# Optimization experiments

Measured on AMD Instinct MI355X. Metric: run time of the kernel, lower is better.

Reference implementation:

```python
import jax, jax.numpy as jnp
import numpy as np

B, S, D = 4, 8192, 512
WS = 512        # window_size
LB = 1          # look_backward (look_forward = 0, causal)


def setup_inputs() -> dict:
    key = jax.random.key(0)
    k1, k2, k3 = jax.random.split(key, 3)
    text = jax.random.normal(k1, (B, S, D), dtype=jnp.float32)
    audio = jax.random.normal(k2, (B, S, D), dtype=jnp.float32)
    video = jax.random.normal(k3, (B, S, D), dtype=jnp.float32)
    return {"text": text, "audio": audio, "video": video}


def _local_attention(q, k, v, ws=WS, lb=LB):
    # q, k, v: [b, n, d]; sliding-window causal attention, each query window
    # attends to its own window plus `lb` previous windows.
    b, n, d = q.shape
    w = n // ws
    scale = d ** -0.5
    qw = q.reshape(b, w, ws, d) * scale
    kw = k.reshape(b, w, ws, d)
    vw = v.reshape(b, w, ws, d)

    def look_around(x):
        # pad lb windows of zeros at the front, gather lb+1 shifted views
        padded = jnp.pad(x, ((0, 0), (lb, 0), (0, 0), (0, 0)))
        return jnp.concatenate([padded[:, i:i + w] for i in range(lb + 1)], axis=2)

    kk = look_around(kw)  # [b, w, (lb+1)*ws, d]
    vv = look_around(vw)

    # absolute positions for causal + padding mask
    t = jnp.arange(n).reshape(w, ws)                        # query positions [w, ws]
    tk = jnp.pad(t, ((lb, 0), (0, 0)), constant_values=-1)  # pad windows get -1
    bq_k = jnp.concatenate([tk[i:i + w] for i in range(lb + 1)], axis=1)  # [w, (lb+1)*ws]
    mask = (t[:, :, None] >= bq_k[:, None, :]) & (bq_k[:, None, :] >= 0)  # [w, ws, (lb+1)*ws]

    sim = jnp.einsum('bwid,bwjd->bwij', qw, kk)             # [b, w, ws, (lb+1)*ws]
    sim = jnp.where(mask[None], sim, jnp.finfo(sim.dtype).min)
    attn = jax.nn.softmax(sim, axis=-1)
    out = jnp.einsum('bwij,bwjd->bwid', attn, vv)
    return out.reshape(b, n, d)


def reference(text, audio, video):
    # GATSBlock.forward: x = self.local_attn(text, audio, video)
    # i.e. q = text, k = audio, v = video (modalities pre-projected to [b, n, d])
    return _local_attention(text, audio, video)
```

## Files before the change

kernel.cpp:

```cpp
#include <hip/hip_runtime.h>
#include <hip/hip_bf16.h>

#define S_ 8192
#define D_ 512
#define WSZ 512
#define QBLK 128
#define KBLK 32
#define ATT_THREADS 512
#define PREG 131072
#define PSTRIDE 2560
#define ATT_LDS (PREG + 4 * PSTRIDE)

using bf16x8 = __attribute__((ext_vector_type(8))) __bf16;
using f32x4  = __attribute__((ext_vector_type(4))) float;
using f32x16 = __attribute__((ext_vector_type(16))) float;

#define GLDS(gp, lp) __builtin_amdgcn_global_load_lds( \
    (const __attribute__((address_space(1))) void*)(gp), \
    (__attribute__((address_space(3))) void*)(lp), 16, 0, 0)

__global__ __launch_bounds__(256) void cvt_k(const float* __restrict__ in,
                                             ushort* __restrict__ out) {
    const int bid = blockIdx.x;
    const int j = bid & 7, t = (bid >> 3) & 255, b = bid >> 11;
    const int u = j * 256 + threadIdx.x;
    const int c = u >> 7, row = (u >> 2) & 31, h = u & 3;
    const float* src = in + ((size_t)(b * S_ + t * 32 + row)) * D_ + c * 32 + h * 8;
    float4 a0 = *(const float4*)(src);
    float4 a1 = *(const float4*)(src + 4);
    bf16x8 o;
    o[0] = (__bf16)a0.x; o[1] = (__bf16)a0.y; o[2] = (__bf16)a0.z; o[3] = (__bf16)a0.w;
    o[4] = (__bf16)a1.x; o[5] = (__bf16)a1.y; o[6] = (__bf16)a1.z; o[7] = (__bf16)a1.w;
    *(bf16x8*)(out + (size_t)(b * 256 + t) * 16384 + u * 8) = o;
}

__global__ __launch_bounds__(256) void tr_v(const float* __restrict__ V,
                                            char* __restrict__ Vt) {
    __shared__ float tile[64][68];
    const int bid = blockIdx.x;
    const int d0 = (bid & 7) * 64;
    const int s0 = ((bid >> 3) & 127) * 64;
    const int b  = bid >> 10;
    const int t  = threadIdx.x;
    {
        const int sl = t >> 2, cg = (t & 3) * 16;
        const float* src = V + ((size_t)b * S_ + s0 + sl) * D_ + d0 + cg;
        #pragma unroll
        for (int j = 0; j < 4; ++j)
            *(float4*)&tile[sl][cg + j * 4] = *(const float4*)(src + j * 4);
    }
    __syncthreads();
    {
        const int dl = t >> 2, sg = (t & 3) * 16;
        const int d  = d0 + dl;
        const int tt = (s0 + sg) >> 5;
        const int kk = (s0 + sg) & 31;
        bf16x8 o0, o1;
        #pragma unroll
        for (int j = 0; j < 8; ++j) {
            o0[j] = (__bf16)tile[sg + j][dl];
            o1[j] = (__bf16)tile[sg + 8 + j][dl];
        }
        char* base = Vt + (size_t)(b * 256 + tt) * 32768 +
                     (d >> 5) * 2048 + (d & 31) * 16;
        *(bf16x8*)(base + (kk >> 4) * 1024)       = o0;
        *(bf16x8*)(base + (kk >> 4) * 1024 + 512) = o1;
    }
}

__global__ __launch_bounds__(ATT_THREADS, 2) void gats_attn(
    const float* __restrict__ Qg, const char* __restrict__ Kbg,
    const char* __restrict__ Vtg, float* __restrict__ Og)
{
    extern __shared__ char smem[];
    const int tid  = threadIdx.x;
    const int lane = tid & 63;
    const int wv   = tid >> 6;
    const int h    = lane >> 4;
    const int lq   = lane & 15;
    const int hh   = lane >> 5;
    const int l31  = lane & 31;
    const int u    = wv & 1;
    const int pr   = wv >> 1;
    char* Pp = smem + PREG + pr * PSTRIDE;
    char* Pf = Pp + 2048;
    const int laneK = lq * 64 + h * 16;

    const int bid = blockIdx.x;
    const int r2  = bid >> 3;
    const int w   = (bid & 7) * 2 + (r2 & 1);
    const int b   = (r2 >> 1) & 3;
    const int y   = r2 >> 3;
    const int qbase    = w * WSZ + y * QBLK;
    const int pairbase = qbase + pr * 32;
    const int wqbase   = qbase + wv * 16;

    const float* Qp  = Qg  + (size_t)b * S_ * D_;
    const char*  Kbp = Kbg + (size_t)b * 256 * 32768;
    const char*  Vtp = Vtg + (size_t)b * 256 * 32768;
    float*       Op  = Og  + (size_t)b * S_ * D_;

    const float scale = 0.044194173824159216f;
    const float L2E   = 1.44269504088896f;

    bf16x8 qf[16];
    {
        const int qrow = wqbase + lq;
        const float* qsrc = Qp + (size_t)qrow * D_ + h * 8;
        #pragma unroll
        for (int c = 0; c < 16; ++c) {
            float4 a0 = *(const float4*)(qsrc + c * 32);
            float4 a1 = *(const float4*)(qsrc + c * 32 + 4);
            bf16x8 q;
            q[0] = (__bf16)(a0.x * scale); q[1] = (__bf16)(a0.y * scale);
            q[2] = (__bf16)(a0.z * scale); q[3] = (__bf16)(a0.w * scale);
            q[4] = (__bf16)(a1.x * scale); q[5] = (__bf16)(a1.y * scale);
            q[6] = (__bf16)(a1.z * scale); q[7] = (__bf16)(a1.w * scale);
            qf[c] = q;
        }
    }

    f32x16 acc[8];
    #pragma unroll
    for (int dt = 0; dt < 8; ++dt)
        #pragma unroll
        for (int rg = 0; rg < 16; ++rg) acc[dt][rg] = 0.f;
    float m_run = -1e30f, l_run = 0.f;

    const int kstart = (w == 0) ? 0 : (w - 1) * WSZ;
    const int ktend  = qbase + QBLK;

    auto STAGE = [&](int bufi, int kt) {
        char* kb = smem + bufi * 65536;
        char* vb = kb + 32768;
        const size_t tb = ((size_t)(kt >> 5)) << 15;
        const char* ksrc = Kbp + tb;
        const char* vsrc = Vtp + tb;
        #pragma unroll
        for (int s2 = 0; s2 < 4; ++s2) {
            const int off = wv * 4096 + s2 * 1024;
            GLDS(ksrc + off + lane * 16, kb + off);
            GLDS(vsrc + off + lane * 16, vb + off);
        }
    };

    STAGE(0, kstart);
    int cur = 0;
    for (int kt = kstart; kt < ktend; kt += KBLK) {
        const bool hasnext = (kt + KBLK) < ktend;
        if (hasnext) {
            STAGE(cur ^ 1, kt + KBLK);
            asm volatile("s_waitcnt vmcnt(8)" ::: "memory");
        } else {
            asm volatile("s_waitcnt vmcnt(0)" ::: "memory");
        }
        __builtin_amdgcn_s_barrier();

        const bool active = (kt <= pairbase + 31);
        char* Ksh = smem + cur * 65536;
        char* Vsh = Ksh + 32768;

        if (active) {
            f32x4 st[2];
            __builtin_amdgcn_s_setprio(1);
            #pragma unroll
            for (int g = 0; g < 2; ++g) {
                f32x4 sa = (f32x4){0.f, 0.f, 0.f, 0.f};
                f32x4 sb = (f32x4){0.f, 0.f, 0.f, 0.f};
                #pragma unroll
                for (int c = 0; c < 16; ++c) {
                    const int byte = c * 2048 + g * 1024 + laneK;
                    bf16x8 kf = *(const bf16x8*)(Ksh + byte);
                    if (c & 1) sb = __builtin_amdgcn_mfma_f32_16x16x32_bf16(kf, qf[c], sb, 0, 0, 0);
                    else       sa = __builtin_amdgcn_mfma_f32_16x16x32_bf16(kf, qf[c], sa, 0, 0, 0);
                }
                st[g] = sa + sb;
            }
            __builtin_amdgcn_s_setprio(0);

            const int qg = wqbase + lq;
            if (kt + 31 > wqbase) {
                #pragma unroll
                for (int g = 0; g < 2; ++g)
                    #pragma unroll
                    for (int r = 0; r < 4; ++r) {
                        const int key = kt + g * 16 + h * 4 + r;
                        if (key > qg) st[g][r] = -1e30f;
                    }
            }

            float own = fmaxf(fmaxf(fmaxf(st[0][0], st[0][1]), fmaxf(st[0][2], st[0][3])),
                              fmaxf(fmaxf(st[1][0], st[1][1]), fmaxf(st[1][2], st[1][3])));
            float tmax = fmaxf(own, __shfl_xor(own, 16));
            tmax = fmaxf(tmax, __shfl_xor(tmax, 32));

            const bool anyneed = __any(tmax > m_run + 8.f);
            float f_val = 1.0f;
            if (anyneed) {
                const float mnew = fmaxf(m_run, tmax);
                f_val = exp2f((m_run - mnew) * L2E);
                m_run = mnew;
                l_run *= f_val;
            }

            const float p00 = exp2f((st[0][0] - m_run) * L2E);
            const float p01 = exp2f((st[0][1] - m_run) * L2E);
            const float p02 = exp2f((st[0][2] - m_run) * L2E);
            const float p03 = exp2f((st[0][3] - m_run) * L2E);
            const float p10 = exp2f((st[1][0] - m_run) * L2E);
            const float p11 = exp2f((st[1][1] - m_run) * L2E);
            const float p12 = exp2f((st[1][2] - m_run) * L2E);
            const float p13 = exp2f((st[1][3] - m_run) * L2E);
            float rs = p00 + p01 + p02 + p03 + p10 + p11 + p12 + p13;
            rs += __shfl_xor(rs, 16);
            rs += __shfl_xor(rs, 32);
            l_run += rs;

            uint c0, c1, c2, c3;
            asm("v_cvt_pk_bf16_f32 %0, %1, %2" : "=v"(c0) : "v"(p00), "v"(p01));
            asm("v_cvt_pk_bf16_f32 %0, %1, %2" : "=v"(c1) : "v"(p02), "v"(p03));
            asm("v_cvt_pk_bf16_f32 %0, %1, %2" : "=v"(c2) : "v"(p10), "v"(p11));
            asm("v_cvt_pk_bf16_f32 %0, %1, %2" : "=v"(c3) : "v"(p12), "v"(p13));
            const int wbase = (h >> 1) * 512 + (h & 1) * 8 + (u * 16 + lq) * 16;
            *(uint*)(Pp + wbase)            = c0;
            *(uint*)(Pp + wbase + 4)        = c1;
            *(uint*)(Pp + 1024 + wbase)     = c2;
            *(uint*)(Pp + 1024 + wbase + 4) = c3;
            if (h == 0)    *(float*)(Pf + (u * 16 + lq) * 4) = f_val;
            if (lane == 0) *(uint*)(Pf + 128 + u * 4) = anyneed ? 1u : 0u;
        }

        asm volatile("s_waitcnt lgkmcnt(0)" ::: "memory");
        __builtin_amdgcn_sched_barrier(0);
        __builtin_amdgcn_s_barrier();

        if (active) {
            const uint2 fl = *(const uint2*)(Pf + 128);
            if (fl.x | fl.y) {
                f32x4 fr[4];
                #pragma unroll
                for (int i = 0; i < 4; ++i)
                    fr[i] = *(const f32x4*)(Pf + i * 32 + hh * 16);
                #pragma unroll
                for (int dt = 0; dt < 8; ++dt)
                    #pragma unroll
                    for (int rg = 0; rg < 16; ++rg)
                        acc[dt][rg] *= fr[rg >> 2][rg & 3];
            }

            bf16x8 pa0 = *(const bf16x8*)(Pp + hh * 512 + l31 * 16);
            bf16x8 pa1 = *(const bf16x8*)(Pp + 1024 + hh * 512 + l31 * 16);
            __builtin_amdgcn_s_setprio(1);
            #pragma unroll
            for (int dt = 0; dt < 8; ++dt) {
                const int vb = (u * 8 + dt) * 2048 + hh * 512 + l31 * 16;
                bf16x8 v0 = *(const bf16x8*)(Vsh + vb);
                bf16x8 v1 = *(const bf16x8*)(Vsh + vb + 1024);
                acc[dt] = __builtin_amdgcn_mfma_f32_32x32x16_bf16(pa0, v0, acc[dt], 0, 0, 0);
                acc[dt] = __builtin_amdgcn_mfma_f32_32x32x16_bf16(pa1, v1, acc[dt], 0, 0, 0);
            }
            __builtin_amdgcn_s_setprio(0);
        }
        __builtin_amdgcn_s_barrier();
        cur ^= 1;
    }

    if (h == 0) *(float*)(Pf + (u * 16 + lq) * 4) = l_run;
    asm volatile("s_waitcnt lgkmcnt(0)" ::: "memory");
    __builtin_amdgcn_s_barrier();
    f32x4 iv[4];
    #pragma unroll
    for (int i = 0; i < 4; ++i) {
        f32x4 lv = *(const f32x4*)(Pf + i * 32 + hh * 16);
        iv[i][0] = 1.0f / lv[0]; iv[i][1] = 1.0f / lv[1];
        iv[i][2] = 1.0f / lv[2]; iv[i][3] = 1.0f / lv[3];
    }
    #pragma unroll
    for (int dt = 0; dt < 8; ++dt) {
        const int colb = u * 256 + dt * 32 + l31;
        #pragma unroll
        for (int rg = 0; rg < 16; ++rg) {
            const int row = pairbase + (rg & 3) + 8 * (rg >> 2) + 4 * hh;
            Op[(size_t)row * D_ + colb] = acc[dt][rg] * iv[rg >> 2][rg & 3];
        }
    }
}

#define FB_LDS (32768 + 32768 + 4 * 1024)
__global__ __launch_bounds__(256, 2) void gats_attn_fb(
    const float* __restrict__ Qg, const float* __restrict__ Kg,
    const float* __restrict__ Vg, float* __restrict__ Og)
{
    extern __shared__ char smem[];
    char* Ksh = smem;
    char* Vsh = smem + 32768;
    const int tid  = threadIdx.x;
    const int lane = tid & 63;
    const int wv   = tid >> 6;
    char* Psh = smem + 65536 + wv * 1024;
    const int bid = blockIdx.x;
    const int wh  = bid & 7;
    const int r2  = bid >> 3;
    const int w   = wh * 2 + (r2 & 1);
    const int b   = (r2 >> 1) & 3;
    const int y   = r2 >> 3;
    const int qbase  = w * WSZ + y * 64;
    const int wqbase = qbase + wv * 16;
    const size_t boff = (size_t)b * S_ * D_;
    const float* Qp = Qg + boff; const float* Kp = Kg + boff;
    const float* Vp = Vg + boff; float* Op = Og + boff;
    const float scale = 0.044194173824159216f;
    const float L2E   = 1.44269504088896f;
    bf16x8 qf[16];
    {
        const int qrow = wqbase + (lane & 15);
        const float* qsrc = Qp + (size_t)qrow * D_ + ((lane >> 4) * 8);
        #pragma unroll
        for (int c = 0; c < 16; ++c) {
            float4 a0 = *(const float4*)(qsrc + c * 32);
            float4 a1 = *(const float4*)(qsrc + c * 32 + 4);
            bf16x8 q;
            q[0] = (__bf16)(a0.x * scale); q[1] = (__bf16)(a0.y * scale);
            q[2] = (__bf16)(a0.z * scale); q[3] = (__bf16)(a0.w * scale);
            q[4] = (__bf16)(a1.x * scale); q[5] = (__bf16)(a1.y * scale);
            q[6] = (__bf16)(a1.z * scale); q[7] = (__bf16)(a1.w * scale);
            qf[c] = q;
        }
    }
    f32x4 acc[32];
    #pragma unroll
    for (int i = 0; i < 32; ++i) acc[i] = (f32x4){0.f, 0.f, 0.f, 0.f};
    float m_r[4], l_r[4];
    #pragma unroll
    for (int r = 0; r < 4; ++r) { m_r[r] = -1e30f; l_r[r] = 0.f; }
    const int kstart = (w == 0) ? 0 : (w - 1) * WSZ;
    const int ktend  = qbase + 64;
    for (int kt = kstart; kt < ktend; kt += 32) {
        __syncthreads();
        #pragma unroll
        for (int s = 0; s < 8; ++s) {
            const int row = s * 4 + wv;
            const int dof = lane * 8;
            const float4* src = (const float4*)(Kp + (size_t)(kt + row) * D_ + dof);
            float4 a0 = src[0], a1 = src[1];
            bf16x8 kv;
            kv[0] = (__bf16)a0.x; kv[1] = (__bf16)a0.y; kv[2] = (__bf16)a0.z; kv[3] = (__bf16)a0.w;
            kv[4] = (__bf16)a1.x; kv[5] = (__bf16)a1.y; kv[6] = (__bf16)a1.z; kv[7] = (__bf16)a1.w;
            const int byte = row * 1024 + ((dof * 2) ^ ((row & 7) << 4));
            *(bf16x8*)(Ksh + byte) = kv;
        }
        #pragma unroll
        for (int hh2 = 0; hh2 < 2; ++hh2) {
            const int d = tid + hh2 * 256;
            #pragma unroll
            for (int it = 0; it < 4; ++it) {
                float vvv[8];
                #pragma unroll
                for (int j = 0; j < 8; ++j)
                    vvv[j] = Vp[(size_t)(kt + it * 8 + j) * D_ + d];
                bf16x8 vb;
                #pragma unroll
                for (int j = 0; j < 8; ++j) vb[j] = (__bf16)vvv[j];
                const int byte = d * 64 + ((it * 16) ^ (((d >> 1) & 3) << 4));
                *(bf16x8*)(Vsh + byte) = vb;
            }
        }
        __syncthreads();
        if (kt > wqbase + 15) continue;
        f32x4 sacc[2];
        #pragma unroll
        for (int g = 0; g < 2; ++g) {
            f32x4 s = (f32x4){0.f, 0.f, 0.f, 0.f};
            const int keyrow = g * 16 + (lane & 15);
            #pragma unroll
            for (int c = 0; c < 16; ++c) {
                const int byte = keyrow * 1024 +
                                 ((c * 64 + (lane >> 4) * 16) ^ ((keyrow & 7) << 4));
                bf16x8 kf = *(const bf16x8*)(Ksh + byte);
                s = __builtin_amdgcn_mfma_f32_16x16x32_bf16(qf[c], kf, s, 0, 0, 0);
            }
            sacc[g] = s;
        }
        #pragma unroll
        for (int g = 0; g < 2; ++g) {
            if (kt + g * 16 + 15 > wqbase) {
                const int kg = kt + g * 16 + (lane & 15);
                #pragma unroll
                for (int r = 0; r < 4; ++r) {
                    const int qrow = wqbase + (lane >> 4) * 4 + r;
                    if (kg > qrow) sacc[g][r] = -1e30f;
                }
            }
        }
        float tmax[4];
        #pragma unroll
        for (int r = 0; r < 4; ++r) {
            float v = fmaxf(sacc[0][r], sacc[1][r]);
            #pragma unroll
            for (int off = 8; off >= 1; off >>= 1)
                v = fmaxf(v, __shfl_xor(v, off));
            tmax[r] = v;
        }
        bool need = false;
        #pragma unroll
        for (int r = 0; r < 4; ++r) need |= (tmax[r] > m_r[r] + 8.f);
        if (__any(need)) {
            #pragma unroll
            for (int r = 0; r < 4; ++r) {
                const float mnew = fmaxf(m_r[r], tmax[r]);
                const float f = exp2f((m_r[r] - mnew) * L2E);
                m_r[r] = mnew; l_r[r] *= f;
                #pragma unroll
                for (int dc = 0; dc < 32; ++dc) acc[dc][r] *= f;
            }
        }
        float rsum[4] = {0.f, 0.f, 0.f, 0.f};
        #pragma unroll
        for (int g = 0; g < 2; ++g) {
            #pragma unroll
            for (int r = 0; r < 4; ++r) {
                const float p = exp2f((sacc[g][r] - m_r[r]) * L2E);
                rsum[r] += p;
                const int prow = (lane >> 4) * 4 + r;
                const int byte = prow * 64 +
                                 ((g * 32 + (lane & 15) * 2) ^ (((prow >> 1) & 3) << 4));
                *(__bf16*)(Psh + byte) = (__bf16)p;
            }
        }
        #pragma unroll
        for (int r = 0; r < 4; ++r) {
            float v = rsum[r];
            #pragma unroll
            for (int off = 8; off >= 1; off >>= 1)
                v += __shfl_xor(v, off);
            l_r[r] += v;
        }
        {
            const int prow  = lane & 15;
            const int pbyte = prow * 64 +
                              (((lane >> 4) * 16) ^ (((prow >> 1) & 3) << 4));
            bf16x8 pa = *(const bf16x8*)(Psh + pbyte);
            #pragma unroll
            for (int dc = 0; dc < 32; ++dc) {
                const int d = dc * 16 + (lane & 15);
                const int vbyte = d * 64 +
                                  (((lane >> 4) * 16) ^ (((d >> 1) & 3) << 4));
                bf16x8 vf = *(const bf16x8*)(Vsh + vbyte);
                acc[dc] = __builtin_amdgcn_mfma_f32_16x16x32_bf16(pa, vf, acc[dc], 0, 0, 0);
            }
        }
    }
    float inv[4];
    #pragma unroll
    for (int r = 0; r < 4; ++r) inv[r] = 1.0f / l_r[r];
    #pragma unroll
    for (int dc = 0; dc < 32; ++dc) {
        #pragma unroll
        for (int r = 0; r < 4; ++r) {
            const int row = wqbase + (lane >> 4) * 4 + r;
            const int col = dc * 16 + (lane & 15);
            Op[(size_t)row * D_ + col] = acc[dc][r] * inv[r];
        }
    }
}

extern "C" void kernel_launch(void* const* d_in, const int* in_sizes, int n_in,
                              void* d_out, int out_size, void* d_ws, size_t ws_size,
                              hipStream_t stream) {
    const float* q = (const float*)d_in[0];
    const float* k = (const float*)d_in[1];
    const float* v = (const float*)d_in[2];
    float* o = (float*)d_out;

    const size_t elems = (size_t)4 * S_ * D_ * 4;
    const size_t need  = elems * 2 * 2;
    if (ws_size >= need) {
        char* kb = (char*)d_ws;
        char* vt = (char*)d_ws + elems * 2;
        cvt_k<<<dim3(8192), dim3(256), 0, stream>>>(k, (ushort*)kb);
        tr_v <<<dim3(4096), dim3(256), 0, stream>>>(v, vt);
        hipFuncSetAttribute((const void*)gats_attn,
                            hipFuncAttributeMaxDynamicSharedMemorySize, ATT_LDS);
        gats_attn<<<dim3(256), dim3(ATT_THREADS), ATT_LDS, stream>>>(q, kb, vt, o);
    } else {
        hipFuncSetAttribute((const void*)gats_attn_fb,
                            hipFuncAttributeMaxDynamicSharedMemorySize, FB_LDS);
        gats_attn_fb<<<dim3(512), dim3(256), FB_LDS, stream>>>(q, k, v, o);
    }
}
```

Measured before the change: 147.2 us.

## Split QK^T over head dim across wave pair and exchange partial scores via LDS

Each wave in a pair now computes QK^T partial scores for both 16-row query blocks of the pair over half of the head dimension. Each K fragment read from LDS therefore feeds two MFMAs, halving per-wave K LDS traffic and Q register footprint. The partial sums are exchanged through a new LDS region and combined, which adds an extra barrier per key tile, more LDS usage per block, and extra LDS writes and reads.

```diff
diff --git a/kernel.cpp b/kernel.cpp
--- a/kernel.cpp
+++ b/kernel.cpp
@@ -8,7 +8,7 @@
 #define KBLK 32
 #define ATT_THREADS 512
 #define PREG 131072
-#define PSTRIDE 2560
+#define PSTRIDE 6400
 #define ATT_LDS (PREG + 4 * PSTRIDE)
 
 using bf16x8 = __attribute__((ext_vector_type(8))) __bf16;
@@ -82,7 +82,8 @@
     const int l31  = lane & 31;
     const int u    = wv & 1;
     const int pr   = wv >> 1;
-    char* Pp = smem + PREG + pr * PSTRIDE;
+    char* Ex = smem + PREG + pr * PSTRIDE;
+    char* Pp = Ex + 4096;
     char* Pf = Pp + 2048;
     const int laneK = lq * 64 + h * 16;
 
@@ -103,12 +104,13 @@
     const float scale = 0.044194173824159216f;
     const float L2E   = 1.44269504088896f;
 
-    bf16x8 qf[16];
-    {
-        const int qrow = wqbase + lq;
-        const float* qsrc = Qp + (size_t)qrow * D_ + h * 8;
-        #pragma unroll
-        for (int c = 0; c < 16; ++c) {
+    bf16x8 qfm[2][8];
+    #pragma unroll
+    for (int m = 0; m < 2; ++m) {
+        const int qrow = pairbase + m * 16 + lq;
+        const float* qsrc = Qp + (size_t)qrow * D_ + u * 256 + h * 8;
+        #pragma unroll
+        for (int c = 0; c < 8; ++c) {
             float4 a0 = *(const float4*)(qsrc + c * 32);
             float4 a1 = *(const float4*)(qsrc + c * 32 + 4);
             bf16x8 q;
@@ -116,7 +118,7 @@
             q[2] = (__bf16)(a0.z * scale); q[3] = (__bf16)(a0.w * scale);
             q[4] = (__bf16)(a1.x * scale); q[5] = (__bf16)(a1.y * scale);
             q[6] = (__bf16)(a1.z * scale); q[7] = (__bf16)(a1.w * scale);
-            qf[c] = q;
+            qfm[m][c] = q;
         }
     }
 
@@ -161,22 +163,34 @@
         char* Vsh = Ksh + 32768;
 
         if (active) {
+            f32x4 stp[2][2];
+            #pragma unroll
+            for (int g = 0; g < 2; ++g)
+                #pragma unroll
+                for (int m = 0; m < 2; ++m)
+                    stp[g][m] = (f32x4){0.f, 0.f, 0.f, 0.f};
+            __builtin_amdgcn_s_setprio(1);
+            #pragma unroll
+            for (int c = 0; c < 8; ++c) {
+                const int byte = (u * 8 + c) * 2048 + laneK;
+                bf16x8 kf0 = *(const bf16x8*)(Ksh + byte);
+                bf16x8 kf1 = *(const bf16x8*)(Ksh + byte + 1024);
+                stp[0][0] = __builtin_amdgcn_mfma_f32_16x16x32_bf16(kf0, qfm[0][c], stp[0][0], 0, 0, 0);
+                stp[0][1] = __builtin_amdgcn_mfma_f32_16x16x32_bf16(kf0, qfm[1][c], stp[0][1], 0, 0, 0);
+                stp[1][0] = __builtin_amdgcn_mfma_f32_16x16x32_bf16(kf1, qfm[0][c], stp[1][0], 0, 0, 0);
+                stp[1][1] = __builtin_amdgcn_mfma_f32_16x16x32_bf16(kf1, qfm[1][c], stp[1][1], 0, 0, 0);
+            }
+            __builtin_amdgcn_s_setprio(0);
+            *(f32x4*)(Ex + u * 2048 + lane * 16)        = stp[0][1 - u];
+            *(f32x4*)(Ex + u * 2048 + 1024 + lane * 16) = stp[1][1 - u];
+
+            asm volatile("s_waitcnt lgkmcnt(0)" ::: "memory");
+            __builtin_amdgcn_sched_barrier(0);
+            __builtin_amdgcn_s_barrier();
+
             f32x4 st[2];
-            __builtin_amdgcn_s_setprio(1);
-            #pragma unroll
-            for (int g = 0; g < 2; ++g) {
-                f32x4 sa = (f32x4){0.f, 0.f, 0.f, 0.f};
-                f32x4 sb = (f32x4){0.f, 0.f, 0.f, 0.f};
-                #pragma unroll
-                for (int c = 0; c < 16; ++c) {
-                    const int byte = c * 2048 + g * 1024 + laneK;
-                    bf16x8 kf = *(const bf16x8*)(Ksh + byte);
-                    if (c & 1) sb = __builtin_amdgcn_mfma_f32_16x16x32_bf16(kf, qf[c], sb, 0, 0, 0);
-                    else       sa = __builtin_amdgcn_mfma_f32_16x16x32_bf16(kf, qf[c], sa, 0, 0, 0);
-                }
-                st[g] = sa + sb;
-            }
-            __builtin_amdgcn_s_setprio(0);
+            st[0] = stp[0][u] + *(const f32x4*)(Ex + (1 - u) * 2048 + lane * 16);
+            st[1] = stp[1][u] + *(const f32x4*)(Ex + (1 - u) * 2048 + 1024 + lane * 16);
 
             const int qg = wqbase + lq;
             if (kt + 31 > wqbase) {
@@ -228,6 +242,8 @@
             *(uint*)(Pp + 1024 + wbase + 4) = c3;
             if (h == 0)    *(float*)(Pf + (u * 16 + lq) * 4) = f_val;
             if (lane == 0) *(uint*)(Pf + 128 + u * 4) = anyneed ? 1u : 0u;
+        } else {
+            __builtin_amdgcn_s_barrier();
         }
 
         asm volatile("s_waitcnt lgkmcnt(0)" ::: "memory");
```

Result: slower. 216.2 us (+46.8%).

## Software-pipeline PV of previous tile with QK of current tile

Applied to the files above, without the earlier changes.

Restructures the attention loop so the P·V product for the previous key tile runs in the same iteration as the Q·K and softmax for the current tile. The P and V buffers become double-buffered, and K and V are staged separately with different lead times. This removes one block barrier per iteration and lets MFMA work overlap the softmax and exp latency. The cost is an epilogue iteration, more LDS traffic bookkeeping, possible register pressure, and a redundant reload of K on the last iteration.

```diff
diff --git a/kernel.cpp b/kernel.cpp
--- a/kernel.cpp
+++ b/kernel.cpp
@@ -7,9 +7,9 @@
 #define QBLK 128
 #define KBLK 32
 #define ATT_THREADS 512
-#define PREG 131072
-#define PSTRIDE 2560
-#define ATT_LDS (PREG + 4 * PSTRIDE)
+#define PHALF 2304
+#define PSTRIDE (2 * PHALF)
+#define ATT_LDS (131072 + 4 * PSTRIDE)
 
 using bf16x8 = __attribute__((ext_vector_type(8))) __bf16;
 using f32x4  = __attribute__((ext_vector_type(4))) float;
@@ -82,8 +82,7 @@
     const int l31  = lane & 31;
     const int u    = wv & 1;
     const int pr   = wv >> 1;
-    char* Pp = smem + PREG + pr * PSTRIDE;
-    char* Pf = Pp + 2048;
+    char* Ppair = smem + 131072 + pr * PSTRIDE;
     const int laneK = lq * 64 + h * 16;
 
     const int bid = blockIdx.x;
@@ -130,38 +129,42 @@
     const int kstart = (w == 0) ? 0 : (w - 1) * WSZ;
     const int ktend  = qbase + QBLK;
 
-    auto STAGE = [&](int bufi, int kt) {
-        char* kb = smem + bufi * 65536;
-        char* vb = kb + 32768;
-        const size_t tb = ((size_t)(kt >> 5)) << 15;
-        const char* ksrc = Kbp + tb;
-        const char* vsrc = Vtp + tb;
+    auto STAGE_K = [&](int parw, int kt) {
+        char* kb = smem + parw * 32768;
+        const char* ksrc = Kbp + (((size_t)(kt >> 5)) << 15);
         #pragma unroll
         for (int s2 = 0; s2 < 4; ++s2) {
             const int off = wv * 4096 + s2 * 1024;
             GLDS(ksrc + off + lane * 16, kb + off);
+        }
+    };
+    auto STAGE_V = [&](int parw, int kt) {
+        char* vb = smem + 65536 + parw * 32768;
+        const char* vsrc = Vtp + (((size_t)(kt >> 5)) << 15);
+        #pragma unroll
+        for (int s2 = 0; s2 < 4; ++s2) {
+            const int off = wv * 4096 + s2 * 1024;
             GLDS(vsrc + off + lane * 16, vb + off);
         }
     };
 
-    STAGE(0, kstart);
-    int cur = 0;
-    for (int kt = kstart; kt < ktend; kt += KBLK) {
-        const bool hasnext = (kt + KBLK) < ktend;
-        if (hasnext) {
-            STAGE(cur ^ 1, kt + KBLK);
-            asm volatile("s_waitcnt vmcnt(8)" ::: "memory");
-        } else {
-            asm volatile("s_waitcnt vmcnt(0)" ::: "memory");
-        }
+    STAGE_K(0, kstart);
+    int it = 0;
+    bool prev_act = false;
+    for (int kt = kstart; kt < ktend; kt += KBLK, ++it) {
+        const int par   = it & 1;
+        const bool act  = (kt <= pairbase + 31);
+        const int knext = (kt + KBLK < ktend) ? (kt + KBLK) : kt;
+        STAGE_K(par ^ 1, knext);
+        STAGE_V(par, kt);
+        asm volatile("s_waitcnt vmcnt(8)" ::: "memory");
         __builtin_amdgcn_s_barrier();
 
-        const bool active = (kt <= pairbase + 31);
-        char* Ksh = smem + cur * 65536;
-        char* Vsh = Ksh + 32768;
-
-        if (active) {
-            f32x4 st[2];
+        char* Ksh = smem + par * 32768;
+        char* Pw  = Ppair + par * PHALF;
+
+        f32x4 st[2];
+        if (act) {
             __builtin_amdgcn_s_setprio(1);
             #pragma unroll
             for (int g = 0; g < 2; ++g) {
@@ -177,7 +180,38 @@
                 st[g] = sa + sb;
             }
             __builtin_amdgcn_s_setprio(0);
-
+        }
+
+        if (prev_act) {
+            char* Pr = Ppair + (par ^ 1) * PHALF;
+            char* Vr = smem + 65536 + (par ^ 1) * 32768;
+            const uint2 fl = *(const uint2*)(Pr + 2176);
+            if (fl.x | fl.y) {
+                f32x4 fr[4];
+                #pragma unroll
+                for (int i = 0; i < 4; ++i)
+                    fr[i] = *(const f32x4*)(Pr + 2048 + i * 32 + hh * 16);
+                #pragma unroll
+                for (int dt = 0; dt < 8; ++dt)
+                    #pragma unroll
+                    for (int rg = 0; rg < 16; ++rg)
+                        acc[dt][rg] *= fr[rg >> 2][rg & 3];
+            }
+            bf16x8 pa0 = *(const bf16x8*)(Pr + hh * 512 + l31 * 16);
+            bf16x8 pa1 = *(const bf16x8*)(Pr + 1024 + hh * 512 + l31 * 16);
+            __builtin_amdgcn_s_setprio(1);
+            #pragma unroll
+            for (int dt = 0; dt < 8; ++dt) {
+                const int vb = (u * 8 + dt) * 2048 + hh * 512 + l31 * 16;
+                bf16x8 v0 = *(const bf16x8*)(Vr + vb);
+                bf16x8 v1 = *(const bf16x8*)(Vr + vb + 1024);
+                acc[dt] = __builtin_amdgcn_mfma_f32_32x32x16_bf16(pa0, v0, acc[dt], 0, 0, 0);
+                acc[dt] = __builtin_amdgcn_mfma_f32_32x32x16_bf16(pa1, v1, acc[dt], 0, 0, 0);
+            }
+            __builtin_amdgcn_s_setprio(0);
+        }
+
+        if (act) {
             const int qg = wqbase + lq;
             if (kt + 31 > wqbase) {
                 #pragma unroll
@@ -188,7 +222,6 @@
                         if (key > qg) st[g][r] = -1e30f;
                     }
             }
-
             float own = fmaxf(fmaxf(fmaxf(st[0][0], st[0][1]), fmaxf(st[0][2], st[0][3])),
                               fmaxf(fmaxf(st[1][0], st[1][1]), fmaxf(st[1][2], st[1][3])));
             float tmax = fmaxf(own, __shfl_xor(own, 16));
@@ -222,56 +255,60 @@
             asm("v_cvt_pk_bf16_f32 %0, %1, %2" : "=v"(c2) : "v"(p10), "v"(p11));
             asm("v_cvt_pk_bf16_f32 %0, %1, %2" : "=v"(c3) : "v"(p12), "v"(p13));
             const int wbase = (h >> 1) * 512 + (h & 1) * 8 + (u * 16 + lq) * 16;
-            *(uint*)(Pp + wbase)            = c0;
-            *(uint*)(Pp + wbase + 4)        = c1;
-            *(uint*)(Pp + 1024 + wbase)     = c2;
-            *(uint*)(Pp + 1024 + wbase + 4) = c3;
-            if (h == 0)    *(float*)(Pf + (u * 16 + lq) * 4) = f_val;
-            if (lane == 0) *(uint*)(Pf + 128 + u * 4) = anyneed ? 1u : 0u;
+            *(uint*)(Pw + wbase)            = c0;
+            *(uint*)(Pw + wbase + 4)        = c1;
+            *(uint*)(Pw + 1024 + wbase)     = c2;
+            *(uint*)(Pw + 1024 + wbase + 4) = c3;
+            if (h == 0)    *(float*)(Pw + 2048 + (u * 16 + lq) * 4) = f_val;
+            if (lane == 0) *(uint*)(Pw + 2176 + u * 4) = anyneed ? 1u : 0u;
         }
 
         asm volatile("s_waitcnt lgkmcnt(0)" ::: "memory");
         __builtin_amdgcn_sched_barrier(0);
         __builtin_amdgcn_s_barrier();
-
-        if (active) {
-            const uint2 fl = *(const uint2*)(Pf + 128);
+        prev_act = act;
+    }
+
+    {
+        const int lastpar = (it - 1) & 1;
+        asm volatile("s_waitcnt vmcnt(0)" ::: "memory");
+        __builtin_amdgcn_s_barrier();
+        if (prev_act) {
+            char* Pr = Ppair + lastpar * PHALF;
+            char* Vr = smem + 65536 + lastpar * 32768;
+            const uint2 fl = *(const uint2*)(Pr + 2176);
             if (fl.x | fl.y) {
                 f32x4 fr[4];
                 #pragma unroll
                 for (int i = 0; i < 4; ++i)
-                    fr[i] = *(const f32x4*)(Pf + i * 32 + hh * 16);
+                    fr[i] = *(const f32x4*)(Pr + 2048 + i * 32 + hh * 16);
                 #pragma unroll
                 for (int dt = 0; dt < 8; ++dt)
                     #pragma unroll
                     for (int rg = 0; rg < 16; ++rg)
                         acc[dt][rg] *= fr[rg >> 2][rg & 3];
             }
-
-            bf16x8 pa0 = *(const bf16x8*)(Pp + hh * 512 + l31 * 16);
-            bf16x8 pa1 = *(const bf16x8*)(Pp + 1024 + hh * 512 + l31 * 16);
-            __builtin_amdgcn_s_setprio(1);
+            bf16x8 pa0 = *(const bf16x8*)(Pr + hh * 512 + l31 * 16);
+            bf16x8 pa1 = *(const bf16x8*)(Pr + 1024 + hh * 512 + l31 * 16);
             #pragma unroll
             for (int dt = 0; dt < 8; ++dt) {
                 const int vb = (u * 8 + dt) * 2048 + hh * 512 + l31 * 16;
-                bf16x8 v0 = *(const bf16x8*)(Vsh + vb);
-                bf16x8 v1 = *(const bf16x8*)(Vsh + vb + 1024);
+                bf16x8 v0 = *(const bf16x8*)(Vr + vb);
+                bf16x8 v1 = *(const bf16x8*)(Vr + vb + 1024);
                 acc[dt] = __builtin_amdgcn_mfma_f32_32x32x16_bf16(pa0, v0, acc[dt], 0, 0, 0);
                 acc[dt] = __builtin_amdgcn_mfma_f32_32x32x16_bf16(pa1, v1, acc[dt], 0, 0, 0);
             }
-            __builtin_amdgcn_s_setprio(0);
-        }
-        __builtin_amdgcn_s_barrier();
-        cur ^= 1;
-    }
-
-    if (h == 0) *(float*)(Pf + (u * 16 + lq) * 4) = l_run;
+        }
+    }
+
+    __builtin_amdgcn_s_barrier();
+    if (h == 0) *(float*)(Ppair + 2048 + (u * 16 + lq) * 4) = l_run;
     asm volatile("s_waitcnt lgkmcnt(0)" ::: "memory");
     __builtin_amdgcn_s_barrier();
     f32x4 iv[4];
     #pragma unroll
     for (int i = 0; i < 4; ++i) {
-        f32x4 lv = *(const f32x4*)(Pf + i * 32 + hh * 16);
+        f32x4 lv = *(const f32x4*)(Ppair + 2048 + i * 32 + hh * 16);
         iv[i][0] = 1.0f / lv[0]; iv[i][1] = 1.0f / lv[1];
         iv[i][2] = 1.0f / lv[2]; iv[i][3] = 1.0f / lv[3];
     }
```

Result: faster. 144.3 us (-2.0%).
